# Performance work log

Hardware: AMD Instinct MI355X
Metric: run time of the kernel (lower is better)

Reference implementation:

```python
import math
import jax, jax.numpy as jnp
import numpy as np

N, T, D, H = 256, 64, 1024, 1024

def setup_inputs() -> dict:
    key = jax.random.key(0)
    ks = jax.random.split(key, 5)
    x = jax.random.normal(ks[0], (N, T, D), dtype=jnp.float32)
    A = jax.random.normal(ks[1], (N, H, 4, 4), dtype=jnp.float32)
    Wx = jax.random.normal(ks[2], (D, 4 * H), dtype=jnp.float32) / math.sqrt(D)
    Wh = jax.random.normal(ks[3], (H, 4 * H), dtype=jnp.float32) / math.sqrt(H)
    Wattn = jax.random.normal(ks[4], (H, 4 * H), dtype=jnp.float32) / math.sqrt(H)
    b = jnp.zeros((4 * H,), dtype=jnp.float32)
    return {"x": x, "A": A, "Wx": Wx, "Wh": Wh, "Wattn": Wattn, "b": b}

def reference(x, A, Wx, Wh, Wattn, b):
    n, t, d = x.shape
    h_dim = A.shape[1]
    inv_sqrt_h = 1.0 / math.sqrt(h_dim)
    A_flat = A.reshape(n, h_dim, 16)  # (N, H, 16 spatial positions)
    h0 = A_flat.mean(axis=2)
    c0 = h0

    def step(carry, x_t):
        prev_h, prev_c = carry
        # scaled dot-product attention over 4x4 grid
        scores = jnp.einsum("nh,nhp->np", prev_h, A_flat) * inv_sqrt_h  # (N,16)
        w = jax.nn.softmax(scores, axis=1)
        attn = jnp.einsum("nhp,np->nh", A_flat, w)  # (N,H)
        # fused LSTM gates
        a = x_t @ Wx + prev_h @ Wh + attn @ Wattn + b  # (N,4H)
        a_i, a_f, a_o, a_g = jnp.split(a, 4, axis=1)
        next_c = jax.nn.sigmoid(a_f) * prev_c + jax.nn.sigmoid(a_i) * jnp.tanh(a_g)
        next_h = jax.nn.sigmoid(a_o) * jnp.tanh(next_c)
        return (next_h, next_c), next_h

    xs = jnp.transpose(x, (1, 0, 2))  # (T,N,D)
    _, hs = jax.lax.scan(step, (h0, c0), xs)
    hn = jnp.transpose(hs, (1, 0, 2))  # (N,T,H)
    return hn
```

## Files before the change

kernel.cpp:

```cpp
#include <hip/hip_runtime.h>

#define N_ 256
#define T_ 64
#define D_ 1024
#define H_ 1024
#define G_ 4096
#define P_ 16
#define KTOT 3072
#define INV_SQRT_H 0.03125f
#define KSPLIT 8
#define KPB 384

typedef __attribute__((ext_vector_type(8))) short short8_t;
typedef __attribute__((ext_vector_type(4))) float f32x4;

__device__ __forceinline__ unsigned short f2bf(float f) {
    unsigned int u = __float_as_uint(f);
    unsigned int r = (u + 0x7FFFu + ((u >> 16) & 1u)) >> 16;
    return (unsigned short)r;
}
__device__ __forceinline__ float bf2f(unsigned short h) {
    return __uint_as_float(((unsigned int)h) << 16);
}
__device__ __forceinline__ float fsig(float x) { return 1.0f / (1.0f + __expf(-x)); }
__device__ __forceinline__ float ftanh(float x) { return 1.0f - 2.0f / (__expf(2.0f * x) + 1.0f); }

__device__ __forceinline__ void gl_lds16(const void* g, void* l) {
    __builtin_amdgcn_global_load_lds(
        (const __attribute__((address_space(1))) unsigned int*)g,
        (__attribute__((address_space(3))) unsigned int*)l, 16, 0, 0);
}

__global__ __launch_bounds__(256) void prep_weights(
    const float* __restrict__ Wx, const float* __restrict__ Wh,
    const float* __restrict__ Wattn,
    unsigned short* __restrict__ WT_hi, unsigned short* __restrict__ WT_lo)
{
    __shared__ float tr[64][65];
    const int tid = threadIdx.x;
    const int j0 = blockIdx.x * 64;
    const int k0 = blockIdx.y * 64;
    const int mat = blockIdx.z;
    const float* src = (mat == 0) ? Wx : (mat == 1) ? Wh : Wattn;
    const int koff = mat * 1024;

    #pragma unroll
    for (int l = 0; l < 4; ++l) {
        const int flat = l * 256 + tid;
        const int kk = flat >> 4;
        const int jj4 = (flat & 15) * 4;
        float4 v = *(const float4*)(src + (size_t)(k0 + kk) * G_ + j0 + jj4);
        tr[kk][jj4] = v.x; tr[kk][jj4 + 1] = v.y; tr[kk][jj4 + 2] = v.z; tr[kk][jj4 + 3] = v.w;
    }
    __syncthreads();
    #pragma unroll
    for (int l = 0; l < 8; ++l) {
        const int flat = l * 256 + tid;
        const int jj = flat >> 5;
        const int kk = (flat & 31) * 2;
        float v0 = tr[kk][jj], v1 = tr[kk + 1][jj];
        size_t o = (size_t)(j0 + jj) * KTOT + koff + k0 + kk;
        ushort2 h, lo;
        h.x = f2bf(v0); h.y = f2bf(v1);
        lo.x = f2bf(v0 - bf2f(h.x)); lo.y = f2bf(v1 - bf2f(h.y));
        *(ushort2*)&WT_hi[o] = h;
        *(ushort2*)&WT_lo[o] = lo;
    }
}

__global__ __launch_bounds__(256) void prep_x(
    const float* __restrict__ x,
    unsigned short* __restrict__ Xhi, unsigned short* __restrict__ Xlo)
{
    const int n = blockIdx.x, t = blockIdx.y, tid = threadIdx.x;
    const size_t o = ((size_t)n * T_ + t) * D_ + tid * 4;
    float4 v = *(const float4*)(x + o);
    ushort4 hi, lo;
    hi.x = f2bf(v.x); lo.x = f2bf(v.x - bf2f(hi.x));
    hi.y = f2bf(v.y); lo.y = f2bf(v.y - bf2f(hi.y));
    hi.z = f2bf(v.z); lo.z = f2bf(v.z - bf2f(hi.z));
    hi.w = f2bf(v.w); lo.w = f2bf(v.w - bf2f(hi.w));
    *(ushort4*)&Xhi[o] = hi;
    *(ushort4*)&Xlo[o] = lo;
}

__global__ __launch_bounds__(256) void init_kernel(
    const float* __restrict__ A,
    float* __restrict__ c_buf,
    unsigned short* __restrict__ ha_hi, unsigned short* __restrict__ ha_lo)
{
    const int n = blockIdx.x, tid = threadIdx.x;
    const int m0 = tid * 4;
    const float* An = A + (size_t)n * H_ * P_;
    __shared__ float sred[4][P_];
    __shared__ float wsh[P_];

    float ar[4][P_];
    float hv[4];
    float sc[P_];
    #pragma unroll
    for (int p = 0; p < P_; ++p) sc[p] = 0.0f;

    #pragma unroll
    for (int r = 0; r < 4; ++r) {
        const float4* row = (const float4*)(An + (size_t)(m0 + r) * P_);
        float4 v0 = row[0], v1 = row[1], v2 = row[2], v3 = row[3];
        ar[r][0]=v0.x; ar[r][1]=v0.y; ar[r][2]=v0.z; ar[r][3]=v0.w;
        ar[r][4]=v1.x; ar[r][5]=v1.y; ar[r][6]=v1.z; ar[r][7]=v1.w;
        ar[r][8]=v2.x; ar[r][9]=v2.y; ar[r][10]=v2.z; ar[r][11]=v2.w;
        ar[r][12]=v3.x; ar[r][13]=v3.y; ar[r][14]=v3.z; ar[r][15]=v3.w;
        float s = 0.0f;
        #pragma unroll
        for (int p = 0; p < P_; ++p) s += ar[r][p];
        hv[r] = s * (1.0f / 16.0f);
        #pragma unroll
        for (int p = 0; p < P_; ++p) sc[p] += hv[r] * ar[r][p];
    }
    float4 c4; c4.x = hv[0]; c4.y = hv[1]; c4.z = hv[2]; c4.w = hv[3];
    *(float4*)(c_buf + (size_t)n * H_ + m0) = c4;
    ushort4 hh, hl;
    hh.x=f2bf(hv[0]); hh.y=f2bf(hv[1]); hh.z=f2bf(hv[2]); hh.w=f2bf(hv[3]);
    hl.x=f2bf(hv[0]-bf2f(hh.x)); hl.y=f2bf(hv[1]-bf2f(hh.y));
    hl.z=f2bf(hv[2]-bf2f(hh.z)); hl.w=f2bf(hv[3]-bf2f(hh.w));
    *(ushort4*)&ha_hi[(size_t)n * 2048 + m0] = hh;
    *(ushort4*)&ha_lo[(size_t)n * 2048 + m0] = hl;

    #pragma unroll
    for (int off = 32; off > 0; off >>= 1)
        #pragma unroll
        for (int p = 0; p < P_; ++p) sc[p] += __shfl_down(sc[p], off);
    if ((tid & 63) == 0) {
        #pragma unroll
        for (int p = 0; p < P_; ++p) sred[tid >> 6][p] = sc[p];
    }
    __syncthreads();
    if (tid == 0) {
        float s[P_], m = -1e30f;
        #pragma unroll
        for (int p = 0; p < P_; ++p) {
            s[p] = (sred[0][p] + sred[1][p] + sred[2][p] + sred[3][p]) * INV_SQRT_H;
            m = fmaxf(m, s[p]);
        }
        float sum = 0.0f;
        #pragma unroll
        for (int p = 0; p < P_; ++p) { s[p] = __expf(s[p] - m); sum += s[p]; }
        float inv = 1.0f / sum;
        #pragma unroll
        for (int p = 0; p < P_; ++p) wsh[p] = s[p] * inv;
    }
    __syncthreads();
    float w[P_];
    #pragma unroll
    for (int p = 0; p < P_; ++p) w[p] = wsh[p];
    float at[4];
    #pragma unroll
    for (int r = 0; r < 4; ++r) {
        float a = 0.0f;
        #pragma unroll
        for (int p = 0; p < P_; ++p) a = fmaf(ar[r][p], w[p], a);
        at[r] = a;
    }
    ushort4 th, tl;
    th.x=f2bf(at[0]); th.y=f2bf(at[1]); th.z=f2bf(at[2]); th.w=f2bf(at[3]);
    tl.x=f2bf(at[0]-bf2f(th.x)); tl.y=f2bf(at[1]-bf2f(th.y));
    tl.z=f2bf(at[2]-bf2f(th.z)); tl.w=f2bf(at[3]-bf2f(th.w));
    *(ushort4*)&ha_hi[(size_t)n * 2048 + 1024 + m0] = th;
    *(ushort4*)&ha_lo[(size_t)n * 2048 + 1024 + m0] = tl;
}

__global__ __launch_bounds__(256) void gemm_kernel(
    const unsigned short* __restrict__ Xhi, const unsigned short* __restrict__ Xlo, int t,
    const unsigned short* __restrict__ ha_hi, const unsigned short* __restrict__ ha_lo,
    const unsigned short* __restrict__ WT_hi, const unsigned short* __restrict__ WT_lo,
    float* __restrict__ parts)
{
    __shared__ unsigned short Ahi[128][32], Alo[128][32], Bhi[128][32], Blo[128][32];
    const int tid = threadIdx.x;
    const int j0 = blockIdx.x * 128;
    const int n0 = blockIdx.y * 128;
    const int kz = blockIdx.z;
    const int w = tid >> 6, lane = tid & 63;
    const int wm = w & 1, wn = w >> 1;
    const int quad = lane >> 4, l15 = lane & 15;
    const int lrow = lane >> 2;
    const int gchunk = (lane & 3) ^ (lrow & 3);

    f32x4 acc[4][4];
    #pragma unroll
    for (int mt = 0; mt < 4; ++mt)
        #pragma unroll
        for (int nt = 0; nt < 4; ++nt) acc[mt][nt] = (f32x4){0.f, 0.f, 0.f, 0.f};

    for (int ks = 0; ks < KPB / 32; ++ks) {
        const int kglob = kz * KPB + ks * 32;
        const int phase0 = (kglob < 1024);
        const unsigned short* pAhi;
        const unsigned short* pAlo;
        size_t rstride, coff;
        if (phase0) {
            pAhi = Xhi + (size_t)t * D_;  pAlo = Xlo + (size_t)t * D_;
            rstride = (size_t)T_ * D_;    coff = kglob;
        } else {
            pAhi = ha_hi;  pAlo = ha_lo;
            rstride = 2048;               coff = kglob - 1024;
        }

        __syncthreads();
        #pragma unroll
        for (int i = 0; i < 2; ++i) {
            const int row = w * 32 + i * 16 + lrow;
            const int rb = w * 32 + i * 16;
            gl_lds16(pAhi + (size_t)(n0 + row) * rstride + coff + gchunk * 8, &Ahi[rb][0]);
            gl_lds16(pAlo + (size_t)(n0 + row) * rstride + coff + gchunk * 8, &Alo[rb][0]);
            gl_lds16(WT_hi + (size_t)(j0 + row) * KTOT + kglob + gchunk * 8, &Bhi[rb][0]);
            gl_lds16(WT_lo + (size_t)(j0 + row) * KTOT + kglob + gchunk * 8, &Blo[rb][0]);
        }
        __syncthreads();

        short8_t bh[4], bl[4];
        #pragma unroll
        for (int nt = 0; nt < 4; ++nt) {
            const int jr = wn * 64 + nt * 16 + l15;
            const int c = (quad ^ (jr & 3)) * 8;
            bh[nt] = *(const short8_t*)&Bhi[jr][c];
            bl[nt] = *(const short8_t*)&Blo[jr][c];
        }
        #pragma unroll
        for (int mt = 0; mt < 4; ++mt) {
            const int mr = wm * 64 + mt * 16 + l15;
            const int c = (quad ^ (mr & 3)) * 8;
            short8_t ah = *(const short8_t*)&Ahi[mr][c];
            short8_t al = *(const short8_t*)&Alo[mr][c];
            #pragma unroll
            for (int nt = 0; nt < 4; ++nt) {
                acc[mt][nt] = __builtin_amdgcn_mfma_f32_16x16x32_bf16(al, bh[nt], acc[mt][nt], 0, 0, 0);
                acc[mt][nt] = __builtin_amdgcn_mfma_f32_16x16x32_bf16(ah, bl[nt], acc[mt][nt], 0, 0, 0);
                acc[mt][nt] = __builtin_amdgcn_mfma_f32_16x16x32_bf16(ah, bh[nt], acc[mt][nt], 0, 0, 0);
            }
        }
    }

    #pragma unroll
    for (int mt = 0; mt < 4; ++mt) {
        const int r0 = n0 + wm * 64 + mt * 16 + quad * 4;
        #pragma unroll
        for (int nt = 0; nt < 4; ++nt) {
            const int cc = j0 + wn * 64 + nt * 16 + l15;
            #pragma unroll
            for (int reg = 0; reg < 4; ++reg)
                parts[((size_t)kz * N_ + r0 + reg) * G_ + cc] = acc[mt][nt][reg];
        }
    }
}

__global__ __launch_bounds__(256) void gates_kernel(
    const float* __restrict__ parts, const float* __restrict__ bvec,
    const float* __restrict__ A, float* __restrict__ c_buf,
    unsigned short* __restrict__ ha_hi, unsigned short* __restrict__ ha_lo,
    float* __restrict__ out, int t)
{
    const int n = blockIdx.x, tid = threadIdx.x;
    const int m0 = tid * 4;
    const float* An = A + (size_t)n * H_ * P_;
    __shared__ float sred[4][P_];
    __shared__ float wsh[P_];

    float ar[4][P_];
    #pragma unroll
    for (int r = 0; r < 4; ++r) {
        const float4* row = (const float4*)(An + (size_t)(m0 + r) * P_);
        float4 v0 = row[0], v1 = row[1], v2 = row[2], v3 = row[3];
        ar[r][0]=v0.x; ar[r][1]=v0.y; ar[r][2]=v0.z; ar[r][3]=v0.w;
        ar[r][4]=v1.x; ar[r][5]=v1.y; ar[r][6]=v1.z; ar[r][7]=v1.w;
        ar[r][8]=v2.x; ar[r][9]=v2.y; ar[r][10]=v2.z; ar[r][11]=v2.w;
        ar[r][12]=v3.x; ar[r][13]=v3.y; ar[r][14]=v3.z; ar[r][15]=v3.w;
    }

    float ga[4][4];
    #pragma unroll
    for (int g = 0; g < 4; ++g) {
        const int j = g * 1024 + m0;
        float4 s = *(const float4*)(bvec + j);
        #pragma unroll
        for (int z = 0; z < KSPLIT; ++z) {
            float4 p = *(const float4*)(parts + ((size_t)z * N_ + n) * G_ + j);
            s.x += p.x; s.y += p.y; s.z += p.z; s.w += p.w;
        }
        ga[g][0] = s.x; ga[g][1] = s.y; ga[g][2] = s.z; ga[g][3] = s.w;
    }

    float4 c4 = *(const float4*)(c_buf + (size_t)n * H_ + m0);
    float cold[4] = {c4.x, c4.y, c4.z, c4.w};
    float nh[4], ncv[4];
    #pragma unroll
    for (int r = 0; r < 4; ++r) {
        float nc = fsig(ga[1][r]) * cold[r] + fsig(ga[0][r]) * ftanh(ga[3][r]);
        ncv[r] = nc;
        nh[r] = fsig(ga[2][r]) * ftanh(nc);
    }
    float4 co; co.x = ncv[0]; co.y = ncv[1]; co.z = ncv[2]; co.w = ncv[3];
    *(float4*)(c_buf + (size_t)n * H_ + m0) = co;
    float4 ho; ho.x = nh[0]; ho.y = nh[1]; ho.z = nh[2]; ho.w = nh[3];
    *(float4*)(out + ((size_t)n * T_ + t) * H_ + m0) = ho;
    ushort4 hh, hl;
    hh.x=f2bf(nh[0]); hh.y=f2bf(nh[1]); hh.z=f2bf(nh[2]); hh.w=f2bf(nh[3]);
    hl.x=f2bf(nh[0]-bf2f(hh.x)); hl.y=f2bf(nh[1]-bf2f(hh.y));
    hl.z=f2bf(nh[2]-bf2f(hh.z)); hl.w=f2bf(nh[3]-bf2f(hh.w));
    *(ushort4*)&ha_hi[(size_t)n * 2048 + m0] = hh;
    *(ushort4*)&ha_lo[(size_t)n * 2048 + m0] = hl;

    float sc[P_];
    #pragma unroll
    for (int p = 0; p < P_; ++p) {
        float s = 0.0f;
        #pragma unroll
        for (int r = 0; r < 4; ++r) s = fmaf(nh[r], ar[r][p], s);
        sc[p] = s;
    }
    #pragma unroll
    for (int off = 32; off > 0; off >>= 1)
        #pragma unroll
        for (int p = 0; p < P_; ++p) sc[p] += __shfl_down(sc[p], off);
    if ((tid & 63) == 0) {
        #pragma unroll
        for (int p = 0; p < P_; ++p) sred[tid >> 6][p] = sc[p];
    }
    __syncthreads();
    if (tid == 0) {
        float s[P_], m = -1e30f;
        #pragma unroll
        for (int p = 0; p < P_; ++p) {
            s[p] = (sred[0][p] + sred[1][p] + sred[2][p] + sred[3][p]) * INV_SQRT_H;
            m = fmaxf(m, s[p]);
        }
        float sum = 0.0f;
        #pragma unroll
        for (int p = 0; p < P_; ++p) { s[p] = __expf(s[p] - m); sum += s[p]; }
        float inv = 1.0f / sum;
        #pragma unroll
        for (int p = 0; p < P_; ++p) wsh[p] = s[p] * inv;
    }
    __syncthreads();
    float w[P_];
    #pragma unroll
    for (int p = 0; p < P_; ++p) w[p] = wsh[p];
    #pragma unroll
    for (int r = 0; r < 4; ++r) {
        float a = 0.0f;
        #pragma unroll
        for (int p = 0; p < P_; ++p) a = fmaf(ar[r][p], w[p], a);
        unsigned short th = f2bf(a);
        unsigned short tl = f2bf(a - bf2f(th));
        ha_hi[(size_t)n * 2048 + 1024 + m0 + r] = th;
        ha_lo[(size_t)n * 2048 + 1024 + m0 + r] = tl;
    }
}

extern "C" void kernel_launch(void* const* d_in, const int* in_sizes, int n_in,
                              void* d_out, int out_size, void* d_ws, size_t ws_size,
                              hipStream_t stream) {
    const float* x     = (const float*)d_in[0];
    const float* A     = (const float*)d_in[1];
    const float* Wx    = (const float*)d_in[2];
    const float* Wh    = (const float*)d_in[3];
    const float* Wattn = (const float*)d_in[4];
    const float* b     = (const float*)d_in[5];
    float* out = (float*)d_out;

    unsigned short* WT_hi = (unsigned short*)d_ws;
    unsigned short* WT_lo = WT_hi + (size_t)G_ * KTOT;
    unsigned short* Xhi   = WT_lo + (size_t)G_ * KTOT;
    unsigned short* Xlo   = Xhi + (size_t)N_ * T_ * D_;
    unsigned short* ha_hi = Xlo + (size_t)N_ * T_ * D_;
    unsigned short* ha_lo = ha_hi + (size_t)N_ * 2048;
    float* c_buf = (float*)(ha_lo + (size_t)N_ * 2048);
    float* parts = c_buf + (size_t)N_ * H_;

    prep_weights<<<dim3(64, 16, 3), 256, 0, stream>>>(Wx, Wh, Wattn, WT_hi, WT_lo);
    prep_x<<<dim3(N_, T_), 256, 0, stream>>>(x, Xhi, Xlo);
    init_kernel<<<N_, 256, 0, stream>>>(A, c_buf, ha_hi, ha_lo);

    for (int t = 0; t < T_; ++t) {
        gemm_kernel<<<dim3(32, 2, KSPLIT), 256, 0, stream>>>(
            Xhi, Xlo, t, ha_hi, ha_lo, WT_hi, WT_lo, parts);
        gates_kernel<<<N_, 256, 0, stream>>>(parts, b, A, c_buf, ha_hi, ha_lo, out, t);
    }
}
```

Before: 2.530 ms.

## Double-buffer LDS tiles in the split-K GEMM and widen prep_x per thread

The per-step GEMM now keeps two LDS buffers and issues the global-to-LDS loads for the next K slice before computing the current one, with a single barrier per iteration. This is meant to hide global load latency behind the MFMA work. It doubles shared memory per block to 64KB, which may reduce occupancy. prep_x is also relaunched with 4096 blocks, each thread converting 16 floats instead of 4.

```diff
diff --git a/kernel.cpp b/kernel.cpp
--- a/kernel.cpp
+++ b/kernel.cpp
@@ -72,16 +72,19 @@
     const float* __restrict__ x,
     unsigned short* __restrict__ Xhi, unsigned short* __restrict__ Xlo)
 {
-    const int n = blockIdx.x, t = blockIdx.y, tid = threadIdx.x;
-    const size_t o = ((size_t)n * T_ + t) * D_ + tid * 4;
-    float4 v = *(const float4*)(x + o);
-    ushort4 hi, lo;
-    hi.x = f2bf(v.x); lo.x = f2bf(v.x - bf2f(hi.x));
-    hi.y = f2bf(v.y); lo.y = f2bf(v.y - bf2f(hi.y));
-    hi.z = f2bf(v.z); lo.z = f2bf(v.z - bf2f(hi.z));
-    hi.w = f2bf(v.w); lo.w = f2bf(v.w - bf2f(hi.w));
-    *(ushort4*)&Xhi[o] = hi;
-    *(ushort4*)&Xlo[o] = lo;
+    const size_t base = ((size_t)blockIdx.x * 256 + threadIdx.x) * 16;
+    #pragma unroll
+    for (int i = 0; i < 4; ++i) {
+        const size_t o = base + i * 4;
+        float4 v = *(const float4*)(x + o);
+        ushort4 hi, lo;
+        hi.x = f2bf(v.x); lo.x = f2bf(v.x - bf2f(hi.x));
+        hi.y = f2bf(v.y); lo.y = f2bf(v.y - bf2f(hi.y));
+        hi.z = f2bf(v.z); lo.z = f2bf(v.z - bf2f(hi.z));
+        hi.w = f2bf(v.w); lo.w = f2bf(v.w - bf2f(hi.w));
+        *(ushort4*)&Xhi[o] = hi;
+        *(ushort4*)&Xlo[o] = lo;
+    }
 }
 
 __global__ __launch_bounds__(256) void init_kernel(
@@ -174,7 +177,7 @@
     const unsigned short* __restrict__ WT_hi, const unsigned short* __restrict__ WT_lo,
     float* __restrict__ parts)
 {
-    __shared__ unsigned short Ahi[128][32], Alo[128][32], Bhi[128][32], Blo[128][32];
+    __shared__ unsigned short buf[2][4][128][32];
     const int tid = threadIdx.x;
     const int j0 = blockIdx.x * 128;
     const int n0 = blockIdx.y * 128;
@@ -191,46 +194,50 @@
         #pragma unroll
         for (int nt = 0; nt < 4; ++nt) acc[mt][nt] = (f32x4){0.f, 0.f, 0.f, 0.f};
 
-    for (int ks = 0; ks < KPB / 32; ++ks) {
+    auto stage = [&](int ks, int bsel) {
         const int kglob = kz * KPB + ks * 32;
-        const int phase0 = (kglob < 1024);
         const unsigned short* pAhi;
         const unsigned short* pAlo;
         size_t rstride, coff;
-        if (phase0) {
+        if (kglob < 1024) {
             pAhi = Xhi + (size_t)t * D_;  pAlo = Xlo + (size_t)t * D_;
             rstride = (size_t)T_ * D_;    coff = kglob;
         } else {
             pAhi = ha_hi;  pAlo = ha_lo;
             rstride = 2048;               coff = kglob - 1024;
         }
-
-        __syncthreads();
         #pragma unroll
         for (int i = 0; i < 2; ++i) {
             const int row = w * 32 + i * 16 + lrow;
             const int rb = w * 32 + i * 16;
-            gl_lds16(pAhi + (size_t)(n0 + row) * rstride + coff + gchunk * 8, &Ahi[rb][0]);
-            gl_lds16(pAlo + (size_t)(n0 + row) * rstride + coff + gchunk * 8, &Alo[rb][0]);
-            gl_lds16(WT_hi + (size_t)(j0 + row) * KTOT + kglob + gchunk * 8, &Bhi[rb][0]);
-            gl_lds16(WT_lo + (size_t)(j0 + row) * KTOT + kglob + gchunk * 8, &Blo[rb][0]);
-        }
-        __syncthreads();
+            gl_lds16(pAhi + (size_t)(n0 + row) * rstride + coff + gchunk * 8, &buf[bsel][0][rb][0]);
+            gl_lds16(pAlo + (size_t)(n0 + row) * rstride + coff + gchunk * 8, &buf[bsel][1][rb][0]);
+            gl_lds16(WT_hi + (size_t)(j0 + row) * KTOT + kglob + gchunk * 8, &buf[bsel][2][rb][0]);
+            gl_lds16(WT_lo + (size_t)(j0 + row) * KTOT + kglob + gchunk * 8, &buf[bsel][3][rb][0]);
+        }
+    };
+
+    stage(0, 0);
+    __syncthreads();
+
+    for (int ks = 0; ks < KPB / 32; ++ks) {
+        const int cur = ks & 1;
+        if (ks + 1 < KPB / 32) stage(ks + 1, cur ^ 1);
 
         short8_t bh[4], bl[4];
         #pragma unroll
         for (int nt = 0; nt < 4; ++nt) {
             const int jr = wn * 64 + nt * 16 + l15;
             const int c = (quad ^ (jr & 3)) * 8;
-            bh[nt] = *(const short8_t*)&Bhi[jr][c];
-            bl[nt] = *(const short8_t*)&Blo[jr][c];
+            bh[nt] = *(const short8_t*)&buf[cur][2][jr][c];
+            bl[nt] = *(const short8_t*)&buf[cur][3][jr][c];
         }
         #pragma unroll
         for (int mt = 0; mt < 4; ++mt) {
             const int mr = wm * 64 + mt * 16 + l15;
             const int c = (quad ^ (mr & 3)) * 8;
-            short8_t ah = *(const short8_t*)&Ahi[mr][c];
-            short8_t al = *(const short8_t*)&Alo[mr][c];
+            short8_t ah = *(const short8_t*)&buf[cur][0][mr][c];
+            short8_t al = *(const short8_t*)&buf[cur][1][mr][c];
             #pragma unroll
             for (int nt = 0; nt < 4; ++nt) {
                 acc[mt][nt] = __builtin_amdgcn_mfma_f32_16x16x32_bf16(al, bh[nt], acc[mt][nt], 0, 0, 0);
@@ -238,6 +245,7 @@
                 acc[mt][nt] = __builtin_amdgcn_mfma_f32_16x16x32_bf16(ah, bh[nt], acc[mt][nt], 0, 0, 0);
             }
         }
+        __syncthreads();
     }
 
     #pragma unroll
@@ -377,7 +385,7 @@
     float* parts = c_buf + (size_t)N_ * H_;
 
     prep_weights<<<dim3(64, 16, 3), 256, 0, stream>>>(Wx, Wh, Wattn, WT_hi, WT_lo);
-    prep_x<<<dim3(N_, T_), 256, 0, stream>>>(x, Xhi, Xlo);
+    prep_x<<<4096, 256, 0, stream>>>(x, Xhi, Xlo);
     init_kernel<<<N_, 256, 0, stream>>>(A, c_buf, ha_hi, ha_lo);
 
     for (int t = 0; t < T_; ++t) {
```

Result: faster. 2.432 ms (-3.9%).
